# Performance work log

Measured on AMD Instinct MI355X. Metric: run time of the kernel, lower is better.

Reference implementation:

```python
import jax, jax.numpy as jnp
import numpy as np

N_HEADS = 16
N_KV_HEADS = 4
N_EMBD = 1024

def setup_inputs() -> dict:
    key = jax.random.key(0)
    kx, kq, kk, kv, ko = jax.random.split(key, 5)
    B, S, E = 2, 2048, N_EMBD
    head_dim = E // N_HEADS
    kv_dim = N_KV_HEADS * head_dim  # 256
    scale = 0.02
    return {
        "x": jax.random.normal(kx, (B, S, E), dtype=jnp.float32),
        "Wq": jax.random.normal(kq, (E, E), dtype=jnp.float32) * scale,
        "Wk": jax.random.normal(kk, (E, kv_dim), dtype=jnp.float32) * scale,
        "Wv": jax.random.normal(kv, (E, kv_dim), dtype=jnp.float32) * scale,
        "Wo": jax.random.normal(ko, (E, E), dtype=jnp.float32) * scale,
    }

def reference(x, Wq, Wk, Wv, Wo):
    B, S, E = x.shape
    H, KV = N_HEADS, N_KV_HEADS
    D = E // H            # head_dim = 64
    R = H // KV           # query heads per kv head = 4
    inv_sqrt_d = 1.0 / (D ** 0.5)

    q = (x @ Wq).reshape(B, S, KV, R, D)   # group query heads by kv group
    k = (x @ Wk).reshape(B, S, KV, D)
    v = (x @ Wv).reshape(B, S, KV, D)

    # repeat_interleave(kv, R, dim=heads) == broadcast kv head g to query heads (g, r)
    scores = jnp.einsum('bqgrd,bkgd->bgrqk', q, k) * inv_sqrt_d  # [B,KV,R,S,S]
    causal = jnp.tril(jnp.ones((S, S), dtype=bool))
    scores = jnp.where(causal, scores, jnp.float32(-jnp.inf))
    attn = jax.nn.softmax(scores, axis=-1)

    out = jnp.einsum('bgrqk,bkgd->bqgrd', attn, v).reshape(B, S, E)
    return out @ Wo
```

## Files before the change

### kernel.cpp

```cpp
#include <hip/hip_runtime.h>
#include <hip/hip_bf16.h>

#define B_SZ   2
#define S_LEN  2048
#define E_DIM  1024
#define H_Q    16
#define H_KV   4
#define HD     64
#define KV_DIM 256
#define M_ROWS (B_SZ * S_LEN)
#define N_QT   (S_LEN / 64)

typedef short bf16x4 __attribute__((ext_vector_type(4)));
typedef short bf16x8 __attribute__((ext_vector_type(8)));
typedef float f32x4  __attribute__((ext_vector_type(4)));
typedef unsigned u32x2 __attribute__((ext_vector_type(2)));

#define MFMA16x32(a, b, c) __builtin_amdgcn_mfma_f32_16x16x32_bf16(a, b, c, 0, 0, 0)

#if __has_builtin(__builtin_amdgcn_mfma_f32_16x16x16bf16_1k)
#define MFMA_PV(a, b, c) __builtin_amdgcn_mfma_f32_16x16x16bf16_1k(a, b, c, 0, 0, 0)
#elif __has_builtin(__builtin_amdgcn_mfma_f32_16x16x16_bf16)
#define MFMA_PV(a, b, c) __builtin_amdgcn_mfma_f32_16x16x16_bf16(a, b, c, 0, 0, 0)
#else
static __device__ inline f32x4 mfma_pv_asm(bf16x4 a, bf16x4 b, f32x4 c) {
    asm volatile("v_mfma_f32_16x16x16_bf16 %0, %1, %2, %0"
                 : "+v"(c) : "v"(a), "v"(b));
    return c;
}
#define MFMA_PV(a, b, c) mfma_pv_asm(a, b, c)
#endif

static __device__ __forceinline__ short f32_to_bf16(float f) {
    unsigned u = __builtin_bit_cast(unsigned, f);
    u += 0x7fffu + ((u >> 16) & 1u);
    return (short)(u >> 16);
}

static __device__ __forceinline__ unsigned pack2_trunc(float a, float b) {
    unsigned ua = __builtin_bit_cast(unsigned, a);
    unsigned ub = __builtin_bit_cast(unsigned, b);
    return (ua >> 16) | (ub & 0xffff0000u);
}

static __device__ __forceinline__ void load_lds16(const short* g, short* l) {
    __builtin_amdgcn_global_load_lds(
        (const __attribute__((address_space(1))) void*)g,
        (__attribute__((address_space(3))) void*)l, 16, 0, 0);
}

__device__ __forceinline__ void transpose_body(const float* __restrict__ W,
                                               short* __restrict__ Wt,
                                               int K, int N, int bx, int by) {
    __shared__ float t[32][33];
    const int n0 = bx * 32, k0 = by * 32;
    const int tx = threadIdx.x & 31, ty = threadIdx.x >> 5;
#pragma unroll
    for (int i = 0; i < 32; i += 8)
        t[ty + i][tx] = W[(long)(k0 + ty + i) * N + n0 + tx];
    __syncthreads();
#pragma unroll
    for (int i = 0; i < 32; i += 8)
        Wt[(long)(n0 + ty + i) * K + k0 + tx] = f32_to_bf16(t[tx][ty + i]);
}

__global__ __launch_bounds__(256)
void prep(const float* __restrict__ x,
          const float* __restrict__ Wq, const float* __restrict__ Wk,
          const float* __restrict__ Wv, const float* __restrict__ Wo,
          short* __restrict__ xbf, short* __restrict__ Wqt,
          short* __restrict__ Wkt, short* __restrict__ Wvt,
          short* __restrict__ Wot) {
    const int bid = blockIdx.x;
    if (bid < 4096) {
        const int i = bid * 256 + threadIdx.x;
        float4 v = ((const float4*)x)[i];
        bf16x4 o;
        o[0] = f32_to_bf16(v.x); o[1] = f32_to_bf16(v.y);
        o[2] = f32_to_bf16(v.z); o[3] = f32_to_bf16(v.w);
        ((bf16x4*)xbf)[i] = o;
    } else if (bid < 5120) {
        const int r = bid - 4096;
        transpose_body(Wq, Wqt, E_DIM, E_DIM, r & 31, r >> 5);
    } else if (bid < 5376) {
        const int r = bid - 5120;
        transpose_body(Wk, Wkt, E_DIM, KV_DIM, r & 7, r >> 3);
    } else if (bid < 5632) {
        const int r = bid - 5376;
        transpose_body(Wv, Wvt, E_DIM, KV_DIM, r & 7, r >> 3);
    } else {
        const int r = bid - 5632;
        transpose_body(Wo, Wot, E_DIM, E_DIM, r & 31, r >> 5);
    }
}

__device__ __forceinline__ void gemm128(const short* __restrict__ Ab,
                                        const short* __restrict__ Btb,
                                        int K, short* As, short* Bs,
                                        f32x4 acc[4][4]) {
    const int tid  = threadIdx.x;
    const int wave = tid >> 6;
    const int lane = tid & 63;
    const int lq   = lane & 15;
    const int lg   = lane >> 4;
    const int wm   = wave >> 1;
    const int wn   = wave & 1;
    const int lrow = lane >> 2;
    const int lkc  = (lane & 3) * 8;

#pragma unroll
    for (int i = 0; i < 4; ++i)
#pragma unroll
        for (int j = 0; j < 4; ++j) acc[i][j] = (f32x4){0.f, 0.f, 0.f, 0.f};

    for (int k0 = 0; k0 < K; k0 += 32) {
        __syncthreads();
#pragma unroll
        for (int it = 0; it < 2; ++it) {
            const int m0 = wave * 32 + it * 16;
            const int m  = m0 + lrow;
            load_lds16(Ab  + (size_t)m * K + k0 + lkc, As + m0 * 32);
            load_lds16(Btb + (size_t)m * K + k0 + lkc, Bs + m0 * 32);
        }
        __syncthreads();
        bf16x8 af[4], bfr[4];
#pragma unroll
        for (int i = 0; i < 4; ++i) {
            af[i]  = *(const bf16x8*)&As[(wm * 64 + i * 16 + lq) * 32 + lg * 8];
            bfr[i] = *(const bf16x8*)&Bs[(wn * 64 + i * 16 + lq) * 32 + lg * 8];
        }
#pragma unroll
        for (int i = 0; i < 4; ++i)
#pragma unroll
            for (int j = 0; j < 4; ++j)
                acc[i][j] = MFMA16x32(af[i], bfr[j], acc[i][j]);
    }
}

__global__ __launch_bounds__(256)
void qkv_gemm(const short* __restrict__ xbf,
              const short* __restrict__ Wqt, const short* __restrict__ Wkt,
              const short* __restrict__ Wvt,
              short* __restrict__ Qbf, short* __restrict__ Kbf,
              short* __restrict__ Vtg, float qscale) {
    __shared__ short As[128 * 32];
    __shared__ short Bs[128 * 32];
    const int nb = blockIdx.x;
    const int mb = blockIdx.y;
    const short* Bt;
    if (nb < 8)       Bt = Wqt + (size_t)nb * 128 * E_DIM;
    else if (nb < 10) Bt = Wkt + (size_t)(nb - 8) * 128 * E_DIM;
    else              Bt = Wvt + (size_t)(nb - 10) * 128 * E_DIM;

    f32x4 acc[4][4];
    gemm128(xbf + (size_t)mb * 128 * E_DIM, Bt, E_DIM, As, Bs, acc);

    const int lane = threadIdx.x & 63, wave = threadIdx.x >> 6;
    const int lq = lane & 15, lg = lane >> 4, wm = wave >> 1, wn = wave & 1;

    if (nb < 10) {
        short* out; int ldc, ncol0; float alpha;
        if (nb < 8) { out = Qbf; ldc = E_DIM; ncol0 = nb * 128; alpha = qscale; }
        else { out = Kbf; ldc = KV_DIM; ncol0 = (nb - 8) * 128; alpha = 1.f; }
#pragma unroll
        for (int i = 0; i < 4; ++i)
#pragma unroll
            for (int r = 0; r < 4; ++r) {
                const size_t row =
                    (size_t)mb * 128 + wm * 64 + i * 16 + lg * 4 + r;
#pragma unroll
                for (int j = 0; j < 4; ++j)
                    out[row * ldc + ncol0 + wn * 64 + j * 16 + lq] =
                        f32_to_bf16(acc[i][j][r] * alpha);
            }
    } else {
        const int ncol0 = (nb - 10) * 128;
#pragma unroll
        for (int i = 0; i < 4; ++i)
#pragma unroll
            for (int r = 0; r < 4; ++r) {
                const int row = mb * 128 + wm * 64 + i * 16 + lg * 4 + r;
                const int bb = row >> 11, s = row & 2047;
#pragma unroll
                for (int j = 0; j < 4; ++j) {
                    const int col = ncol0 + wn * 64 + j * 16 + lq;
                    const int gg = col >> 6, d = col & 63;
                    Vtg[((long)(gg * 2 + bb) * HD + d) * S_LEN + s] =
                        f32_to_bf16(acc[i][j][r]);
                }
            }
    }
}

__global__ __launch_bounds__(256)
void gemm_o(const short* __restrict__ Abf, const short* __restrict__ Wot,
            float* __restrict__ C) {
    __shared__ short As[128 * 32];
    __shared__ short Bs[128 * 32];
    const int nb = blockIdx.x;
    const int mb = blockIdx.y;
    f32x4 acc[4][4];
    gemm128(Abf + (size_t)mb * 128 * E_DIM,
            Wot + (size_t)nb * 128 * E_DIM, E_DIM, As, Bs, acc);

    const int lane = threadIdx.x & 63, wave = threadIdx.x >> 6;
    const int lq = lane & 15, lg = lane >> 4, wm = wave >> 1, wn = wave & 1;
#pragma unroll
    for (int i = 0; i < 4; ++i)
#pragma unroll
        for (int r = 0; r < 4; ++r) {
            const size_t row = (size_t)mb * 128 + wm * 64 + i * 16 + lg * 4 + r;
#pragma unroll
            for (int j = 0; j < 4; ++j)
                C[row * E_DIM + nb * 128 + wn * 64 + j * 16 + lq] =
                    acc[i][j][r];
        }
}

struct KVregs { bf16x8 k[2], v[2]; };

__device__ __forceinline__ void stage_load(const short* __restrict__ Kb,
                                           const short* __restrict__ Vtg,
                                           long b, long ks, int g,
                                           KVregs& kv) {
    const int tid = threadIdx.x;
#pragma unroll
    for (int it = 0; it < 2; ++it) {
        const int c   = tid + it * 256;
        const int row = c >> 3;
        const int ch  = c & 7;
        kv.k[it] = *(const bf16x8*)
            &Kb[(b * S_LEN + ks + row) * KV_DIM + g * HD + ch * 8];
        kv.v[it] = *(const bf16x8*)
            &Vtg[((long)(g * 2 + b) * HD + row) * S_LEN + ks + ch * 8];
    }
}

__device__ __forceinline__ void stage_write(short (*Ks)[72], short (*Vt)[72],
                                            const KVregs& kv) {
    const int tid = threadIdx.x;
#pragma unroll
    for (int it = 0; it < 2; ++it) {
        const int c   = tid + it * 256;
        const int row = c >> 3;
        const int ch  = c & 7;
        *(bf16x8*)&Ks[row][ch * 8] = kv.k[it];
        *(bf16x8*)&Vt[row][ch * 8] = kv.v[it];
    }
}

__global__ __launch_bounds__(256)
void flash_mfma(const short* __restrict__ Qb,
                const short* __restrict__ Kb,
                const short* __restrict__ Vtg,
                float* __restrict__ Op,
                float* __restrict__ Lp) {
    const int pair  = blockIdx.x;
    const int h     = blockIdx.y;
    const int b     = blockIdx.z >> 1;
    const int split = blockIdx.z & 1;
    const int g     = h >> 2;

    const int tid  = threadIdx.x;
    const int wave = tid >> 6;
    const int lane = tid & 63;
    const int lq   = lane & 15;
    const int lg   = lane >> 4;

    __shared__ short Ks[2][64][72];
    __shared__ short Vt[2][64][72];

    for (int rep = 0; rep < 2; ++rep) {
        const int qt = rep ? (N_QT - 1 - pair) : pair;
        const int qs = qt * 64;
        const int half = (qt + 1) >> 1;
        const int kt0  = split ? half : 0;
        const int kt1  = split ? qt : half - 1;

        const short* qrow =
            Qb + ((long)(b * S_LEN + qs + wave * 16 + lq)) * E_DIM + h * HD;
        const bf16x8 qf0 = *(const bf16x8*)(qrow + lg * 8);
        const bf16x8 qf1 = *(const bf16x8*)(qrow + 32 + lg * 8);

        f32x4 o[4];
#pragma unroll
        for (int dc = 0; dc < 4; ++dc) o[dc] = (f32x4){0.f, 0.f, 0.f, 0.f};
        float l_run = 0.f;

        if (kt0 <= kt1) {
            KVregs kv;
            stage_load(Kb, Vtg, b, (long)kt0 * 64, g, kv);
            stage_write(Ks[0], Vt[0], kv);
            __syncthreads();

            int p = 0;
            for (int kt = kt0; kt <= kt1; ++kt) {
                if (kt < kt1)
                    stage_load(Kb, Vtg, b, (long)(kt + 1) * 64, g, kv);

                const int cmax = (kt == qt) ? wave : 3;
                f32x4 s[4];
#pragma unroll
                for (int c = 0; c < 4; ++c) {
                    if (c > cmax) continue;
                    bf16x8 kf0 = *(const bf16x8*)&Ks[p][c * 16 + lq][lg * 8];
                    bf16x8 kf1 =
                        *(const bf16x8*)&Ks[p][c * 16 + lq][32 + lg * 8];
                    f32x4 acc = (f32x4){0.f, 0.f, 0.f, 0.f};
                    acc = MFMA16x32(kf0, qf0, acc);
                    acc = MFMA16x32(kf1, qf1, acc);
                    s[c] = acc;
                }

                if (kt == qt) {
#pragma unroll
                    for (int r = 0; r < 4; ++r)
                        if (lg * 4 + r > lq) s[wave][r] = -INFINITY;
                }

                float psum = 0.f;
#pragma unroll
                for (int c = 0; c < 4; ++c) {
                    if (c > cmax) continue;
#pragma unroll
                    for (int r = 0; r < 4; ++r) {
                        float pe = exp2f(s[c][r]);
                        s[c][r] = pe;
                        psum += pe;
                    }
                }
                l_run += psum;

#pragma unroll
                for (int c = 0; c < 4; ++c) {
                    if (c > cmax) continue;
                    u32x2 packed;
                    packed[0] = pack2_trunc(s[c][0], s[c][1]);
                    packed[1] = pack2_trunc(s[c][2], s[c][3]);
                    bf16x4 pa = __builtin_bit_cast(bf16x4, packed);
#pragma unroll
                    for (int dc = 0; dc < 4; ++dc) {
                        bf16x4 vf = *(const bf16x4*)
                            &Vt[p][dc * 16 + lq][c * 16 + lg * 4];
                        o[dc] = MFMA_PV(pa, vf, o[dc]);
                    }
                }

                if (kt < kt1) stage_write(Ks[p ^ 1], Vt[p ^ 1], kv);
                __syncthreads();
                p ^= 1;
            }
        }

        l_run += __shfl_xor(l_run, 16);
        l_run += __shfl_xor(l_run, 32);

        const long ibase = (long)(split * 2 + b) << 21;
#pragma unroll
        for (int r = 0; r < 4; ++r) {
            const long base = ibase +
                ((long)(qs + wave * 16 + lg * 4 + r)) * E_DIM + h * HD + lq;
#pragma unroll
            for (int dc = 0; dc < 4; ++dc) Op[base + dc * 16] = o[dc][r];
        }
        if (lg == 0)
            Lp[((split * 2 + b) * H_Q + h) * S_LEN + qs + wave * 16 + lq] =
                l_run;
    }
}

__global__ __launch_bounds__(256)
void merge_o(const float* __restrict__ Op, const float* __restrict__ Lp,
             short* __restrict__ Abf) {
    const long idx4 = (long)blockIdx.x * 256 + threadIdx.x;
    const long e = idx4 * 4;
    const int b  = (int)(e >> 21);
    const long ei = e & ((1L << 21) - 1);
    const int s  = (int)(ei >> 10);
    const int hh = ((int)(ei & 1023)) >> 6;
    const float4 v0 = *(const float4*)(Op + ((long)(0 + b) << 21) + ei);
    const float4 v1 = *(const float4*)(Op + ((long)(2 + b) << 21) + ei);
    const float l = Lp[((0 + b) * H_Q + hh) * S_LEN + s] +
                    Lp[((2 + b) * H_Q + hh) * S_LEN + s];
    const float inv = 1.f / l;
    bf16x4 o;
    o[0] = f32_to_bf16((v0.x + v1.x) * inv);
    o[1] = f32_to_bf16((v0.y + v1.y) * inv);
    o[2] = f32_to_bf16((v0.z + v1.z) * inv);
    o[3] = f32_to_bf16((v0.w + v1.w) * inv);
    *(bf16x4*)(Abf + e) = o;
}

extern "C" void kernel_launch(void* const* d_in, const int* in_sizes, int n_in,
                              void* d_out, int out_size, void* d_ws, size_t ws_size,
                              hipStream_t stream) {
    const float* x  = (const float*)d_in[0];
    const float* Wq = (const float*)d_in[1];
    const float* Wk = (const float*)d_in[2];
    const float* Wv = (const float*)d_in[3];
    const float* Wo = (const float*)d_in[4];
    float* out = (float*)d_out;

    short* xbf = (short*)d_ws;
    short* Wqt = xbf + (size_t)M_ROWS * E_DIM;
    short* Wkt = Wqt + (size_t)E_DIM * E_DIM;
    short* Wvt = Wkt + (size_t)KV_DIM * E_DIM;
    short* Wot = Wvt + (size_t)KV_DIM * E_DIM;
    short* Qbf = Wot + (size_t)E_DIM * E_DIM;
    short* Kbf = Qbf + (size_t)M_ROWS * E_DIM;
    short* Vtg = Kbf + (size_t)M_ROWS * KV_DIM;
    short* Abf = Vtg + (size_t)8 * HD * S_LEN;
    float* Op  = (float*)(Abf + (size_t)M_ROWS * E_DIM);
    float* Lp  = Op + (size_t)4 * S_LEN * E_DIM;

    const float qscale = 0.125f * 1.44269504088896340736f;

    prep<<<dim3(6656), dim3(256), 0, stream>>>(
        x, Wq, Wk, Wv, Wo, xbf, Wqt, Wkt, Wvt, Wot);
    qkv_gemm<<<dim3(12, M_ROWS / 128), dim3(256), 0, stream>>>(
        xbf, Wqt, Wkt, Wvt, Qbf, Kbf, Vtg, qscale);
    flash_mfma<<<dim3(N_QT / 2, H_Q, 4), dim3(256), 0, stream>>>(
        Qbf, Kbf, Vtg, Op, Lp);
    merge_o<<<dim3(M_ROWS * E_DIM / 4 / 256), dim3(256), 0, stream>>>(
        Op, Lp, Abf);
    gemm_o<<<dim3(E_DIM / 128, M_ROWS / 128), dim3(256), 0, stream>>>(
        Abf, Wot, out);
}
```

Measured before the change: 198.3 us.

## Shrink GEMM tiles to 128x64 and single-buffer flash attention KV LDS

The QKV and output-projection GEMMs now use 128x64 tiles instead of 128x128, doubling the number of blocks so more CUs are busy on this small problem, at the cost of less operand reuse per block. The flash attention kernel drops its double-buffered K/V shared memory for a single buffer. The next tile is still prefetched into registers, but the LDS write now happens between two barriers at the top of each iteration. This cuts LDS use and may raise occupancy, but it adds a barrier per iteration and exposes the LDS write latency.

```diff
diff --git a/kernel.cpp b/kernel.cpp
--- a/kernel.cpp
+++ b/kernel.cpp
@@ -94,22 +94,20 @@
     }
 }
 
-__device__ __forceinline__ void gemm128(const short* __restrict__ Ab,
-                                        const short* __restrict__ Btb,
-                                        int K, short* As, short* Bs,
-                                        f32x4 acc[4][4]) {
+__device__ __forceinline__ void gemm128x64(const short* __restrict__ Ab,
+                                           const short* __restrict__ Btb,
+                                           int K, short* As, short* Bs,
+                                           f32x4 acc[2][4]) {
     const int tid  = threadIdx.x;
     const int wave = tid >> 6;
     const int lane = tid & 63;
     const int lq   = lane & 15;
     const int lg   = lane >> 4;
-    const int wm   = wave >> 1;
-    const int wn   = wave & 1;
     const int lrow = lane >> 2;
     const int lkc  = (lane & 3) * 8;
 
 #pragma unroll
-    for (int i = 0; i < 4; ++i)
+    for (int i = 0; i < 2; ++i)
 #pragma unroll
         for (int j = 0; j < 4; ++j) acc[i][j] = (f32x4){0.f, 0.f, 0.f, 0.f};
 
@@ -118,19 +116,22 @@
 #pragma unroll
         for (int it = 0; it < 2; ++it) {
             const int m0 = wave * 32 + it * 16;
-            const int m  = m0 + lrow;
-            load_lds16(Ab  + (size_t)m * K + k0 + lkc, As + m0 * 32);
-            load_lds16(Btb + (size_t)m * K + k0 + lkc, Bs + m0 * 32);
+            load_lds16(Ab + (size_t)(m0 + lrow) * K + k0 + lkc, As + m0 * 32);
+        }
+        {
+            const int n0 = wave * 16;
+            load_lds16(Btb + (size_t)(n0 + lrow) * K + k0 + lkc, Bs + n0 * 32);
         }
         __syncthreads();
-        bf16x8 af[4], bfr[4];
-#pragma unroll
-        for (int i = 0; i < 4; ++i) {
-            af[i]  = *(const bf16x8*)&As[(wm * 64 + i * 16 + lq) * 32 + lg * 8];
-            bfr[i] = *(const bf16x8*)&Bs[(wn * 64 + i * 16 + lq) * 32 + lg * 8];
-        }
-#pragma unroll
-        for (int i = 0; i < 4; ++i)
+        bf16x8 af[2], bfr[4];
+#pragma unroll
+        for (int i = 0; i < 2; ++i)
+            af[i] = *(const bf16x8*)&As[(wave * 32 + i * 16 + lq) * 32 + lg * 8];
+#pragma unroll
+        for (int j = 0; j < 4; ++j)
+            bfr[j] = *(const bf16x8*)&Bs[(j * 16 + lq) * 32 + lg * 8];
+#pragma unroll
+        for (int i = 0; i < 2; ++i)
 #pragma unroll
             for (int j = 0; j < 4; ++j)
                 acc[i][j] = MFMA16x32(af[i], bfr[j], acc[i][j]);
@@ -144,47 +145,46 @@
               short* __restrict__ Qbf, short* __restrict__ Kbf,
               short* __restrict__ Vtg, float qscale) {
     __shared__ short As[128 * 32];
-    __shared__ short Bs[128 * 32];
+    __shared__ short Bs[64 * 32];
     const int nb = blockIdx.x;
     const int mb = blockIdx.y;
     const short* Bt;
-    if (nb < 8)       Bt = Wqt + (size_t)nb * 128 * E_DIM;
-    else if (nb < 10) Bt = Wkt + (size_t)(nb - 8) * 128 * E_DIM;
-    else              Bt = Wvt + (size_t)(nb - 10) * 128 * E_DIM;
-
-    f32x4 acc[4][4];
-    gemm128(xbf + (size_t)mb * 128 * E_DIM, Bt, E_DIM, As, Bs, acc);
+    if (nb < 16)      Bt = Wqt + (size_t)nb * 64 * E_DIM;
+    else if (nb < 20) Bt = Wkt + (size_t)(nb - 16) * 64 * E_DIM;
+    else              Bt = Wvt + (size_t)(nb - 20) * 64 * E_DIM;
+
+    f32x4 acc[2][4];
+    gemm128x64(xbf + (size_t)mb * 128 * E_DIM, Bt, E_DIM, As, Bs, acc);
 
     const int lane = threadIdx.x & 63, wave = threadIdx.x >> 6;
-    const int lq = lane & 15, lg = lane >> 4, wm = wave >> 1, wn = wave & 1;
-
-    if (nb < 10) {
+    const int lq = lane & 15, lg = lane >> 4;
+
+    if (nb < 20) {
         short* out; int ldc, ncol0; float alpha;
-        if (nb < 8) { out = Qbf; ldc = E_DIM; ncol0 = nb * 128; alpha = qscale; }
-        else { out = Kbf; ldc = KV_DIM; ncol0 = (nb - 8) * 128; alpha = 1.f; }
-#pragma unroll
-        for (int i = 0; i < 4; ++i)
+        if (nb < 16) { out = Qbf; ldc = E_DIM; ncol0 = nb * 64; alpha = qscale; }
+        else { out = Kbf; ldc = KV_DIM; ncol0 = (nb - 16) * 64; alpha = 1.f; }
+#pragma unroll
+        for (int i = 0; i < 2; ++i)
 #pragma unroll
             for (int r = 0; r < 4; ++r) {
                 const size_t row =
-                    (size_t)mb * 128 + wm * 64 + i * 16 + lg * 4 + r;
+                    (size_t)mb * 128 + wave * 32 + i * 16 + lg * 4 + r;
 #pragma unroll
                 for (int j = 0; j < 4; ++j)
-                    out[row * ldc + ncol0 + wn * 64 + j * 16 + lq] =
+                    out[row * ldc + ncol0 + j * 16 + lq] =
                         f32_to_bf16(acc[i][j][r] * alpha);
             }
     } else {
-        const int ncol0 = (nb - 10) * 128;
-#pragma unroll
-        for (int i = 0; i < 4; ++i)
+        const int gg = nb - 20;
+#pragma unroll
+        for (int i = 0; i < 2; ++i)
 #pragma unroll
             for (int r = 0; r < 4; ++r) {
-                const int row = mb * 128 + wm * 64 + i * 16 + lg * 4 + r;
+                const int row = mb * 128 + wave * 32 + i * 16 + lg * 4 + r;
                 const int bb = row >> 11, s = row & 2047;
 #pragma unroll
                 for (int j = 0; j < 4; ++j) {
-                    const int col = ncol0 + wn * 64 + j * 16 + lq;
-                    const int gg = col >> 6, d = col & 63;
+                    const int d = j * 16 + lq;
                     Vtg[((long)(gg * 2 + bb) * HD + d) * S_LEN + s] =
                         f32_to_bf16(acc[i][j][r]);
                 }
@@ -196,24 +196,24 @@
 void gemm_o(const short* __restrict__ Abf, const short* __restrict__ Wot,
             float* __restrict__ C) {
     __shared__ short As[128 * 32];
-    __shared__ short Bs[128 * 32];
+    __shared__ short Bs[64 * 32];
     const int nb = blockIdx.x;
     const int mb = blockIdx.y;
-    f32x4 acc[4][4];
-    gemm128(Abf + (size_t)mb * 128 * E_DIM,
-            Wot + (size_t)nb * 128 * E_DIM, E_DIM, As, Bs, acc);
+    f32x4 acc[2][4];
+    gemm128x64(Abf + (size_t)mb * 128 * E_DIM,
+               Wot + (size_t)nb * 64 * E_DIM, E_DIM, As, Bs, acc);
 
     const int lane = threadIdx.x & 63, wave = threadIdx.x >> 6;
-    const int lq = lane & 15, lg = lane >> 4, wm = wave >> 1, wn = wave & 1;
-#pragma unroll
-    for (int i = 0; i < 4; ++i)
+    const int lq = lane & 15, lg = lane >> 4;
+#pragma unroll
+    for (int i = 0; i < 2; ++i)
 #pragma unroll
         for (int r = 0; r < 4; ++r) {
-            const size_t row = (size_t)mb * 128 + wm * 64 + i * 16 + lg * 4 + r;
+            const size_t row =
+                (size_t)mb * 128 + wave * 32 + i * 16 + lg * 4 + r;
 #pragma unroll
             for (int j = 0; j < 4; ++j)
-                C[row * E_DIM + nb * 128 + wn * 64 + j * 16 + lq] =
-                    acc[i][j][r];
+                C[row * E_DIM + nb * 64 + j * 16 + lq] = acc[i][j][r];
         }
 }
 
@@ -267,8 +267,8 @@
     const int lq   = lane & 15;
     const int lg   = lane >> 4;
 
-    __shared__ short Ks[2][64][72];
-    __shared__ short Vt[2][64][72];
+    __shared__ short Ks[64][72];
+    __shared__ short Vt[64][72];
 
     for (int rep = 0; rep < 2; ++rep) {
         const int qt = rep ? (N_QT - 1 - pair) : pair;
@@ -287,68 +287,61 @@
         for (int dc = 0; dc < 4; ++dc) o[dc] = (f32x4){0.f, 0.f, 0.f, 0.f};
         float l_run = 0.f;
 
-        if (kt0 <= kt1) {
-            KVregs kv;
-            stage_load(Kb, Vtg, b, (long)kt0 * 64, g, kv);
-            stage_write(Ks[0], Vt[0], kv);
+        KVregs kv;
+        if (kt0 <= kt1) stage_load(Kb, Vtg, b, (long)kt0 * 64, g, kv);
+
+        for (int kt = kt0; kt <= kt1; ++kt) {
             __syncthreads();
-
-            int p = 0;
-            for (int kt = kt0; kt <= kt1; ++kt) {
-                if (kt < kt1)
-                    stage_load(Kb, Vtg, b, (long)(kt + 1) * 64, g, kv);
-
-                const int cmax = (kt == qt) ? wave : 3;
-                f32x4 s[4];
-#pragma unroll
-                for (int c = 0; c < 4; ++c) {
-                    if (c > cmax) continue;
-                    bf16x8 kf0 = *(const bf16x8*)&Ks[p][c * 16 + lq][lg * 8];
-                    bf16x8 kf1 =
-                        *(const bf16x8*)&Ks[p][c * 16 + lq][32 + lg * 8];
-                    f32x4 acc = (f32x4){0.f, 0.f, 0.f, 0.f};
-                    acc = MFMA16x32(kf0, qf0, acc);
-                    acc = MFMA16x32(kf1, qf1, acc);
-                    s[c] = acc;
+            stage_write(Ks, Vt, kv);
+            __syncthreads();
+            if (kt < kt1)
+                stage_load(Kb, Vtg, b, (long)(kt + 1) * 64, g, kv);
+
+            const int cmax = (kt == qt) ? wave : 3;
+            f32x4 s[4];
+#pragma unroll
+            for (int c = 0; c < 4; ++c) {
+                if (c > cmax) continue;
+                bf16x8 kf0 = *(const bf16x8*)&Ks[c * 16 + lq][lg * 8];
+                bf16x8 kf1 = *(const bf16x8*)&Ks[c * 16 + lq][32 + lg * 8];
+                f32x4 acc = (f32x4){0.f, 0.f, 0.f, 0.f};
+                acc = MFMA16x32(kf0, qf0, acc);
+                acc = MFMA16x32(kf1, qf1, acc);
+                s[c] = acc;
+            }
+
+            if (kt == qt) {
+#pragma unroll
+                for (int r = 0; r < 4; ++r)
+                    if (lg * 4 + r > lq) s[wave][r] = -INFINITY;
+            }
+
+            float psum = 0.f;
+#pragma unroll
+            for (int c = 0; c < 4; ++c) {
+                if (c > cmax) continue;
+#pragma unroll
+                for (int r = 0; r < 4; ++r) {
+                    float pe = exp2f(s[c][r]);
+                    s[c][r] = pe;
+                    psum += pe;
                 }
-
-                if (kt == qt) {
-#pragma unroll
-                    for (int r = 0; r < 4; ++r)
-                        if (lg * 4 + r > lq) s[wave][r] = -INFINITY;
+            }
+            l_run += psum;
+
+#pragma unroll
+            for (int c = 0; c < 4; ++c) {
+                if (c > cmax) continue;
+                u32x2 packed;
+                packed[0] = pack2_trunc(s[c][0], s[c][1]);
+                packed[1] = pack2_trunc(s[c][2], s[c][3]);
+                bf16x4 pa = __builtin_bit_cast(bf16x4, packed);
+#pragma unroll
+                for (int dc = 0; dc < 4; ++dc) {
+                    bf16x4 vf =
+                        *(const bf16x4*)&Vt[dc * 16 + lq][c * 16 + lg * 4];
+                    o[dc] = MFMA_PV(pa, vf, o[dc]);
                 }
-
-                float psum = 0.f;
-#pragma unroll
-                for (int c = 0; c < 4; ++c) {
-                    if (c > cmax) continue;
-#pragma unroll
-                    for (int r = 0; r < 4; ++r) {
-                        float pe = exp2f(s[c][r]);
-                        s[c][r] = pe;
-                        psum += pe;
-                    }
-                }
-                l_run += psum;
-
-#pragma unroll
-                for (int c = 0; c < 4; ++c) {
-                    if (c > cmax) continue;
-                    u32x2 packed;
-                    packed[0] = pack2_trunc(s[c][0], s[c][1]);
-                    packed[1] = pack2_trunc(s[c][2], s[c][3]);
-                    bf16x4 pa = __builtin_bit_cast(bf16x4, packed);
-#pragma unroll
-                    for (int dc = 0; dc < 4; ++dc) {
-                        bf16x4 vf = *(const bf16x4*)
-                            &Vt[p][dc * 16 + lq][c * 16 + lg * 4];
-                        o[dc] = MFMA_PV(pa, vf, o[dc]);
-                    }
-                }
-
-                if (kt < kt1) stage_write(Ks[p ^ 1], Vt[p ^ 1], kv);
-                __syncthreads();
-                p ^= 1;
             }
         }
 
@@ -417,12 +410,12 @@
 
     prep<<<dim3(6656), dim3(256), 0, stream>>>(
         x, Wq, Wk, Wv, Wo, xbf, Wqt, Wkt, Wvt, Wot);
-    qkv_gemm<<<dim3(12, M_ROWS / 128), dim3(256), 0, stream>>>(
+    qkv_gemm<<<dim3(24, M_ROWS / 128), dim3(256), 0, stream>>>(
         xbf, Wqt, Wkt, Wvt, Qbf, Kbf, Vtg, qscale);
     flash_mfma<<<dim3(N_QT / 2, H_Q, 4), dim3(256), 0, stream>>>(
         Qbf, Kbf, Vtg, Op, Lp);
     merge_o<<<dim3(M_ROWS * E_DIM / 4 / 256), dim3(256), 0, stream>>>(
         Op, Lp, Abf);
-    gemm_o<<<dim3(E_DIM / 128, M_ROWS / 128), dim3(256), 0, stream>>>(
+    gemm_o<<<dim3(E_DIM / 64, M_ROWS / 128), dim3(256), 0, stream>>>(
         Abf, Wot, out);
 }
```

New measurement: 178.9 us. 1.11x faster.
